# Optimization experiments

Measured on AMD Instinct MI355X. Metric: run time of the kernel, lower is better.

## Reference

```python
import jax, jax.numpy as jnp
import numpy as np

LATENT_DIM = 256
CODEBOOK_SIZE = 8192
COMMITMENT_WEIGHT = 0.25
CODEBOOK_WEIGHT = 1.0


def setup_inputs() -> dict:
    key = jax.random.key(0)
    k1, k2 = jax.random.split(key)
    latents = jax.random.normal(k1, (16, 1024, LATENT_DIM), dtype=jnp.float32)
    patch_mask = jnp.ones((16, 1024), dtype=jnp.float32)
    # nn.init.uniform_(codebook.weight, -1/K, 1/K)
    codebook = jax.random.uniform(
        k2, (CODEBOOK_SIZE, LATENT_DIM), dtype=jnp.float32,
        minval=-1.0 / CODEBOOK_SIZE, maxval=1.0 / CODEBOOK_SIZE)
    return {"latents": latents, "patch_mask": patch_mask, "codebook": codebook}


def reference(latents, patch_mask, codebook):
    B, P, D = latents.shape
    flat = latents.reshape(-1, D)  # [N, D]
    # squared euclidean distances [N, K]
    distances = (
        jnp.sum(flat * flat, axis=1, keepdims=True)
        + jnp.sum(codebook * codebook, axis=1)
        - 2.0 * flat @ codebook.T
    )
    symbol_ids = jnp.argmin(distances, axis=1)          # [N]
    quantized = codebook[symbol_ids].reshape(B, P, D)   # [B, P, D]
    symbol_ids = symbol_ids.reshape(B, P)

    st_quantized = latents + jax.lax.stop_gradient(quantized - latents)
    commitment_loss = jnp.mean((latents - jax.lax.stop_gradient(quantized)) ** 2) * COMMITMENT_WEIGHT
    codebook_loss = jnp.mean((quantized - jax.lax.stop_gradient(latents)) ** 2) * CODEBOOK_WEIGHT

    # perplexity: masked codeword usage histogram without materializing one-hot
    denom = jnp.maximum(jnp.sum(patch_mask), 1.0)
    avg_probs = jax.ops.segment_sum(
        patch_mask.reshape(-1), symbol_ids.reshape(-1),
        num_segments=CODEBOOK_SIZE) / denom
    perplexity = jnp.exp(-jnp.sum(avg_probs * jnp.log(avg_probs + 1e-8)))

    return symbol_ids, quantized, st_quantized, commitment_loss, codebook_loss, perplexity
```

## Files before the change

kernel.cpp:

```cpp
#include <hip/hip_runtime.h>
#include <math.h>

#define DD 256
#define KK 8192
#define NN 16384
#define MT 32
#define RPW 8
#define NT 512
#define NCH (KK / NT)
#define DT 8
#define NSL (DD / DT)
#define NEPOCH (NCH * NSL)
#define NBLOCKS (NN / MT)
#define CBUFF 4096
#define RSTRIDE 260

#define OUT_IDS   0
#define OUT_Q     16384
#define OUT_ST    4210688
#define OUT_COMMIT 8404992
#define OUT_CBL    8404993
#define OUT_PERP   8404994

__device__ __forceinline__ void gl2lds16(const float* g, float* l) {
    __builtin_amdgcn_global_load_lds(
        (const __attribute__((address_space(1))) float*)g,
        (__attribute__((address_space(3))) float*)l, 16, 0, 0);
}

__device__ __forceinline__ float rlane(float v, int l) {
    return __int_as_float(__builtin_amdgcn_readlane(__float_as_int(v), l));
}

__device__ __forceinline__ float np_block128_sumsq(const float* p) {
    #pragma clang fp contract(off)
    float r0 = p[0] * p[0], r1 = p[1] * p[1], r2 = p[2] * p[2], r3 = p[3] * p[3];
    float r4 = p[4] * p[4], r5 = p[5] * p[5], r6 = p[6] * p[6], r7 = p[7] * p[7];
    for (int i = 8; i < 128; i += 8) {
        r0 = r0 + p[i + 0] * p[i + 0];
        r1 = r1 + p[i + 1] * p[i + 1];
        r2 = r2 + p[i + 2] * p[i + 2];
        r3 = r3 + p[i + 3] * p[i + 3];
        r4 = r4 + p[i + 4] * p[i + 4];
        r5 = r5 + p[i + 5] * p[i + 5];
        r6 = r6 + p[i + 6] * p[i + 6];
        r7 = r7 + p[i + 7] * p[i + 7];
    }
    return ((r0 + r1) + (r2 + r3)) + ((r4 + r5) + (r6 + r7));
}

__device__ __forceinline__ float np_pairwise256_sumsq(const float* a) {
    #pragma clang fp contract(off)
    float s0 = np_block128_sumsq(a);
    float s1 = np_block128_sumsq(a + 128);
    return s0 + s1;
}

__global__ __launch_bounds__(256) void rowsumsq(const float* __restrict__ A,
                                                float* __restrict__ out) {
    __shared__ __align__(16) float sA[64][RSTRIDE];
    const int tid = threadIdx.x;
    const int base = blockIdx.x * 64;
    #pragma unroll
    for (int i = 0; i < 16; ++i) {
        int g = i * 256 + tid;
        int row = g >> 6, d4 = g & 63;
        float4 v = reinterpret_cast<const float4*>(A)[(size_t)(base + row) * (DD / 4) + d4];
        *reinterpret_cast<float4*>(&sA[row][d4 * 4]) = v;
    }
    __syncthreads();
    if (tid < 64) out[base + tid] = np_pairwise256_sumsq(sA[tid]);
}

__global__ __launch_bounds__(256, 2) void vq_main(const float* __restrict__ X,
                                                  const float* __restrict__ CB,
                                                  const float* __restrict__ c2,
                                                  const float* __restrict__ x2,
                                                  const float* __restrict__ mask,
                                                  float* __restrict__ out,
                                                  float* __restrict__ hist,
                                                  float* __restrict__ partial) {
    __shared__ __align__(16) float sX[8192];
    __shared__ __align__(16) float sC[2 * CBUFF];
    __shared__ int   row_id[MT];
    __shared__ float wsum[4];

    const int tid  = threadIdx.x;
    const int lane = tid & 63;
    const int wid  = tid >> 6;
    const int widu = __builtin_amdgcn_readfirstlane(wid);
    const int block_row = blockIdx.x * MT;

    {
        const unsigned rr = lane & 7u, d4r = lane >> 3;
        #pragma unroll
        for (int k = 0; k < 8; ++k)
            gl2lds16(X + (size_t)(block_row + widu * 8 + rr) * DD + k * 32 + d4r * 4,
                     &sX[(widu * 8 + k) * 256]);
    }

    unsigned coff[4];
    #pragma unroll
    for (int k = 0; k < 4; ++k) {
        unsigned u  = (widu * 4u + (unsigned)k) * 64u + (unsigned)lane;
        unsigned c  = u & 511u;
        unsigned pl = u >> 9;
        coff[k] = c * DD + pl * 4u;
    }
    #pragma unroll
    for (int k = 0; k < 4; ++k)
        gl2lds16(CB + coff[k], &sC[(widu * 4 + k) * 256]);

    float x2r[RPW];
    #pragma unroll
    for (int rr = 0; rr < RPW; ++rr) x2r[rr] = x2[block_row + wid * RPW + rr];

    __syncthreads();

    float best[RPW];
    int   besti[RPW];
    #pragma unroll
    for (int rr = 0; rr < RPW; ++rr) { best[rr] = 3.4e38f; besti[rr] = 0; }

    for (int ch = 0; ch < NCH; ++ch) {
        float c2v[8];
        #pragma unroll
        for (int j = 0; j < 8; ++j) c2v[j] = c2[ch * NT + lane + 64 * j];

        float acc[8][8];
        #pragma unroll
        for (int rr = 0; rr < 8; ++rr)
            #pragma unroll
            for (int j = 0; j < 8; ++j) acc[rr][j] = 0.0f;

        float4 xp;

        #pragma unroll 4
        for (int sl = 0; sl < NSL; ++sl) {
            const int e = ch * NSL + sl;

            if (e + 1 < NEPOCH) {
                const int nch = (e + 1) >> 5, nsl = (e + 1) & 31;
                const float* so = CB + (size_t)nch * (NT * DD) + nsl * DT;
                float* dst = &sC[((e + 1) & 1) * CBUFF];
                #pragma unroll
                for (int k = 0; k < 4; ++k)
                    gl2lds16(so + coff[k], dst + (widu * 4 + k) * 256);
            }

            if ((sl & 3) == 0) {
                const int b = sl >> 2;
                xp = *reinterpret_cast<const float4*>(&sX[(wid * 8 + b) * 256 + lane * 4]);
            }

            const float* cb_ = &sC[(e & 1) * CBUFF] + lane * 4;
            #pragma unroll
            for (int s = 0; s < 2; ++s) {
                const int t = (sl & 3) * 2 + s;
                float4 cc[8];
                #pragma unroll
                for (int j = 0; j < 8; ++j)
                    cc[j] = *reinterpret_cast<const float4*>(cb_ + s * 2048 + j * 256);
                #pragma unroll
                for (int rr = 0; rr < 8; ++rr) {
                    const int rl = t * 8 + rr;
                    const float sx = rlane(xp.x, rl);
                    const float sy = rlane(xp.y, rl);
                    const float sz = rlane(xp.z, rl);
                    const float sw = rlane(xp.w, rl);
                    #pragma unroll
                    for (int j = 0; j < 8; ++j) {
                        acc[rr][j] = fmaf(sx, cc[j].x, acc[rr][j]);
                        acc[rr][j] = fmaf(sy, cc[j].y, acc[rr][j]);
                        acc[rr][j] = fmaf(sz, cc[j].z, acc[rr][j]);
                        acc[rr][j] = fmaf(sw, cc[j].w, acc[rr][j]);
                    }
                }
            }
            __syncthreads();
        }

        #pragma unroll
        for (int rr = 0; rr < 8; ++rr) {
            #pragma unroll
            for (int j = 0; j < 8; ++j) {
                const int col = ch * NT + lane + 64 * j;
                float t1 = x2r[rr] + c2v[j];
                float sc = t1 - 2.0f * acc[rr][j];
                if (sc < best[rr] || (sc == best[rr] && col < besti[rr])) {
                    best[rr] = sc; besti[rr] = col;
                }
            }
        }
    }

    #pragma unroll
    for (int rr = 0; rr < RPW; ++rr) {
        float b = best[rr];
        int  bi = besti[rr];
        #pragma unroll
        for (int m = 32; m > 0; m >>= 1) {
            float b2 = __shfl_xor(b, m, 64);
            int   i2 = __shfl_xor(bi, m, 64);
            if (b2 < b || (b2 == b && i2 < bi)) { b = b2; bi = i2; }
        }
        if (lane == 0) row_id[wid * RPW + rr] = bi;
    }
    __syncthreads();

    if (tid < MT) {
        int bi = row_id[tid];
        out[OUT_IDS + block_row + tid] = (float)bi;
        atomicAdd(&hist[bi], mask[block_row + tid]);
    }

    float msep = 0.0f;
    float* outq  = out + OUT_Q;
    float* outst = out + OUT_ST;
    #pragma unroll
    for (int i = 0; i < 8; ++i) {
        int g = i * 256 + tid;
        int row = g >> 6;
        int d4  = g & 63;
        int id  = row_id[row];
        float4 q = reinterpret_cast<const float4*>(CB)[(size_t)id * (DD / 4) + d4];
        float4 x = reinterpret_cast<const float4*>(X)[(size_t)(block_row + row) * (DD / 4) + d4];
        float4 st;
        st.x = x.x + (q.x - x.x);
        st.y = x.y + (q.y - x.y);
        st.z = x.z + (q.z - x.z);
        st.w = x.w + (q.w - x.w);
        float dx = x.x - q.x; msep = fmaf(dx, dx, msep);
        dx = x.y - q.y; msep = fmaf(dx, dx, msep);
        dx = x.z - q.z; msep = fmaf(dx, dx, msep);
        dx = x.w - q.w; msep = fmaf(dx, dx, msep);
        size_t o = (size_t)(block_row + row) * (DD / 4) + d4;
        reinterpret_cast<float4*>(outq)[o]  = q;
        reinterpret_cast<float4*>(outst)[o] = st;
    }
    #pragma unroll
    for (int off = 32; off > 0; off >>= 1) msep += __shfl_down(msep, off, 64);
    if (lane == 0) wsum[wid] = msep;
    __syncthreads();
    if (tid == 0) partial[blockIdx.x] = wsum[0] + wsum[1] + wsum[2] + wsum[3];
}

__global__ __launch_bounds__(256) void vq_finalize(const float* __restrict__ partial,
                                                   const float* __restrict__ hist,
                                                   float* __restrict__ out) {
    __shared__ double red[256];
    const int tid = threadIdx.x;

    double ps = 0.0;
    for (int j = tid; j < NBLOCKS; j += 256) ps += (double)partial[j];
    red[tid] = ps;
    __syncthreads();
    for (int s = 128; s > 0; s >>= 1) {
        if (tid < s) red[tid] += red[tid + s];
        __syncthreads();
    }
    double mse_sum = red[0];
    __syncthreads();

    double hs = 0.0;
    for (int j = tid; j < KK; j += 256) hs += (double)hist[j];
    red[tid] = hs;
    __syncthreads();
    for (int s = 128; s > 0; s >>= 1) {
        if (tid < s) red[tid] += red[tid + s];
        __syncthreads();
    }
    double denom = red[0] > 1.0 ? red[0] : 1.0;
    __syncthreads();

    double ent = 0.0;
    for (int j = tid; j < KK; j += 256) {
        double p = (double)hist[j] / denom;
        ent += p * log(p + 1e-8);
    }
    red[tid] = ent;
    __syncthreads();
    for (int s = 128; s > 0; s >>= 1) {
        if (tid < s) red[tid] += red[tid + s];
        __syncthreads();
    }

    if (tid == 0) {
        double mse = mse_sum / (double)((size_t)NN * DD);
        out[OUT_COMMIT] = (float)(mse * 0.25);
        out[OUT_CBL]    = (float)mse;
        out[OUT_PERP]   = (float)exp(-red[0]);
    }
}

extern "C" void kernel_launch(void* const* d_in, const int* in_sizes, int n_in,
                              void* d_out, int out_size, void* d_ws, size_t ws_size,
                              hipStream_t stream) {
    const float* latents = (const float*)d_in[0];
    const float* mask    = (const float*)d_in[1];
    const float* cb      = (const float*)d_in[2];
    float* out = (float*)d_out;

    float* hist    = (float*)d_ws;
    float* partial = hist + KK;
    float* c2      = partial + NBLOCKS;
    float* x2      = c2 + KK;

    hipMemsetAsync(d_ws, 0, KK * sizeof(float), stream);
    rowsumsq<<<KK / 64, 256, 0, stream>>>(cb, c2);
    rowsumsq<<<NN / 64, 256, 0, stream>>>(latents, x2);
    vq_main<<<NBLOCKS, 256, 0, stream>>>(latents, cb, c2, x2, mask, out, hist, partial);
    vq_finalize<<<1, 256, 0, stream>>>(partial, hist, out);
}
```

Baseline: 1.133 ms.

## Split codebook across two wave groups per block and merge argmin in LDS

```diff
diff --git a/kernel.cpp b/kernel.cpp
--- a/kernel.cpp
+++ b/kernel.cpp
@@ -7,12 +7,12 @@
 #define MT 32
 #define RPW 8
 #define NT 512
-#define NCH (KK / NT)
-#define DT 8
+#define NCHG 8
+#define DT 4
 #define NSL (DD / DT)
-#define NEPOCH (NCH * NSL)
+#define NEPG (NCHG * NSL)
 #define NBLOCKS (NN / MT)
-#define CBUFF 4096
+#define CBUFF 2048
 #define RSTRIDE 260
 
 #define OUT_IDS   0
@@ -72,7 +72,7 @@
     if (tid < 64) out[base + tid] = np_pairwise256_sumsq(sA[tid]);
 }
 
-__global__ __launch_bounds__(256, 2) void vq_main(const float* __restrict__ X,
+__global__ __launch_bounds__(512, 4) void vq_main(const float* __restrict__ X,
                                                   const float* __restrict__ CB,
                                                   const float* __restrict__ c2,
                                                   const float* __restrict__ x2,
@@ -81,7 +81,9 @@
                                                   float* __restrict__ hist,
                                                   float* __restrict__ partial) {
     __shared__ __align__(16) float sX[8192];
-    __shared__ __align__(16) float sC[2 * CBUFF];
+    __shared__ __align__(16) float sC[4 * CBUFF];
+    __shared__ float gbest[2][MT];
+    __shared__ int   gidx[2][MT];
     __shared__ int   row_id[MT];
     __shared__ float wsum[4];
 
@@ -89,31 +91,37 @@
     const int lane = tid & 63;
     const int wid  = tid >> 6;
     const int widu = __builtin_amdgcn_readfirstlane(wid);
+    const int g    = wid >> 2;
+    const int gu   = widu >> 2;
+    const int wg   = wid & 3;
+    const int wgu  = widu & 3;
     const int block_row = blockIdx.x * MT;
 
     {
         const unsigned rr = lane & 7u, d4r = lane >> 3;
-        #pragma unroll
-        for (int k = 0; k < 8; ++k)
-            gl2lds16(X + (size_t)(block_row + widu * 8 + rr) * DD + k * 32 + d4r * 4,
-                     &sX[(widu * 8 + k) * 256]);
-    }
-
-    unsigned coff[4];
-    #pragma unroll
-    for (int k = 0; k < 4; ++k) {
-        unsigned u  = (widu * 4u + (unsigned)k) * 64u + (unsigned)lane;
-        unsigned c  = u & 511u;
-        unsigned pl = u >> 9;
-        coff[k] = c * DD + pl * 4u;
-    }
-    #pragma unroll
-    for (int k = 0; k < 4; ++k)
-        gl2lds16(CB + coff[k], &sC[(widu * 4 + k) * 256]);
+        const int r8 = widu >> 1, h = widu & 1;
+        #pragma unroll
+        for (int k = 0; k < 4; ++k) {
+            const int kk = h * 4 + k;
+            gl2lds16(X + (size_t)(block_row + r8 * 8 + rr) * DD + kk * 32 + d4r * 4,
+                     &sX[(r8 * 8 + kk) * 256]);
+        }
+    }
+
+    unsigned coff[2];
+    #pragma unroll
+    for (int k = 0; k < 2; ++k)
+        coff[k] = ((wgu * 2u + (unsigned)k) * 64u + (unsigned)lane) * DD;
+
+    const float* CBg = CB + (size_t)gu * NCHG * NT * DD;
+    float* sCg = &sC[gu * 2 * CBUFF];
+    #pragma unroll
+    for (int k = 0; k < 2; ++k)
+        gl2lds16(CBg + coff[k], sCg + (wgu * 2 + k) * 256);
 
     float x2r[RPW];
     #pragma unroll
-    for (int rr = 0; rr < RPW; ++rr) x2r[rr] = x2[block_row + wid * RPW + rr];
+    for (int rr = 0; rr < RPW; ++rr) x2r[rr] = x2[block_row + wg * RPW + rr];
 
     __syncthreads();
 
@@ -122,10 +130,11 @@
     #pragma unroll
     for (int rr = 0; rr < RPW; ++rr) { best[rr] = 3.4e38f; besti[rr] = 0; }
 
-    for (int ch = 0; ch < NCH; ++ch) {
+    for (int ch = 0; ch < NCHG; ++ch) {
+        const int chg = g * NCHG + ch;
         float c2v[8];
         #pragma unroll
-        for (int j = 0; j < 8; ++j) c2v[j] = c2[ch * NT + lane + 64 * j];
+        for (int j = 0; j < 8; ++j) c2v[j] = c2[chg * NT + lane + 64 * j];
 
         float acc[8][8];
         #pragma unroll
@@ -135,46 +144,42 @@
 
         float4 xp;
 
-        #pragma unroll 4
+        #pragma unroll 8
         for (int sl = 0; sl < NSL; ++sl) {
             const int e = ch * NSL + sl;
 
-            if (e + 1 < NEPOCH) {
-                const int nch = (e + 1) >> 5, nsl = (e + 1) & 31;
-                const float* so = CB + (size_t)nch * (NT * DD) + nsl * DT;
-                float* dst = &sC[((e + 1) & 1) * CBUFF];
+            if (e + 1 < NEPG) {
+                const int nch = (e + 1) >> 6, nsl = (e + 1) & 63;
+                const float* so = CBg + (size_t)nch * (NT * DD) + nsl * DT;
+                float* dst = sCg + ((e + 1) & 1) * CBUFF;
                 #pragma unroll
-                for (int k = 0; k < 4; ++k)
-                    gl2lds16(so + coff[k], dst + (widu * 4 + k) * 256);
+                for (int k = 0; k < 2; ++k)
+                    gl2lds16(so + coff[k], dst + (wgu * 2 + k) * 256);
             }
 
-            if ((sl & 3) == 0) {
-                const int b = sl >> 2;
-                xp = *reinterpret_cast<const float4*>(&sX[(wid * 8 + b) * 256 + lane * 4]);
-            }
-
-            const float* cb_ = &sC[(e & 1) * CBUFF] + lane * 4;
+            if ((sl & 7) == 0)
+                xp = *reinterpret_cast<const float4*>(
+                        &sX[(wg * 8 + (sl >> 3)) * 256 + lane * 4]);
+
+            const int t = sl & 7;
+            const float* cb_ = sCg + (e & 1) * CBUFF + lane * 4;
+            float4 cc[8];
             #pragma unroll
-            for (int s = 0; s < 2; ++s) {
-                const int t = (sl & 3) * 2 + s;
-                float4 cc[8];
+            for (int j = 0; j < 8; ++j)
+                cc[j] = *reinterpret_cast<const float4*>(cb_ + j * 256);
+            #pragma unroll
+            for (int rr = 0; rr < 8; ++rr) {
+                const int rl = t * 8 + rr;
+                const float sx = rlane(xp.x, rl);
+                const float sy = rlane(xp.y, rl);
+                const float sz = rlane(xp.z, rl);
+                const float sw = rlane(xp.w, rl);
                 #pragma unroll
-                for (int j = 0; j < 8; ++j)
-                    cc[j] = *reinterpret_cast<const float4*>(cb_ + s * 2048 + j * 256);
-                #pragma unroll
-                for (int rr = 0; rr < 8; ++rr) {
-                    const int rl = t * 8 + rr;
-                    const float sx = rlane(xp.x, rl);
-                    const float sy = rlane(xp.y, rl);
-                    const float sz = rlane(xp.z, rl);
-                    const float sw = rlane(xp.w, rl);
-                    #pragma unroll
-                    for (int j = 0; j < 8; ++j) {
-                        acc[rr][j] = fmaf(sx, cc[j].x, acc[rr][j]);
-                        acc[rr][j] = fmaf(sy, cc[j].y, acc[rr][j]);
-                        acc[rr][j] = fmaf(sz, cc[j].z, acc[rr][j]);
-                        acc[rr][j] = fmaf(sw, cc[j].w, acc[rr][j]);
-                    }
+                for (int j = 0; j < 8; ++j) {
+                    acc[rr][j] = fmaf(sx, cc[j].x, acc[rr][j]);
+                    acc[rr][j] = fmaf(sy, cc[j].y, acc[rr][j]);
+                    acc[rr][j] = fmaf(sz, cc[j].z, acc[rr][j]);
+                    acc[rr][j] = fmaf(sw, cc[j].w, acc[rr][j]);
                 }
             }
             __syncthreads();
@@ -184,7 +189,7 @@
         for (int rr = 0; rr < 8; ++rr) {
             #pragma unroll
             for (int j = 0; j < 8; ++j) {
-                const int col = ch * NT + lane + 64 * j;
+                const int col = chg * NT + lane + 64 * j;
                 float t1 = x2r[rr] + c2v[j];
                 float sc = t1 - 2.0f * acc[rr][j];
                 if (sc < best[rr] || (sc == best[rr] && col < besti[rr])) {
@@ -204,43 +209,51 @@
             int   i2 = __shfl_xor(bi, m, 64);
             if (b2 < b || (b2 == b && i2 < bi)) { b = b2; bi = i2; }
         }
-        if (lane == 0) row_id[wid * RPW + rr] = bi;
+        if (lane == 0) {
+            gbest[g][wg * RPW + rr] = b;
+            gidx [g][wg * RPW + rr] = bi;
+        }
     }
     __syncthreads();
 
     if (tid < MT) {
-        int bi = row_id[tid];
+        const float b0 = gbest[0][tid], b1 = gbest[1][tid];
+        const int bi = (b1 < b0) ? gidx[1][tid] : gidx[0][tid];
+        row_id[tid] = bi;
         out[OUT_IDS + block_row + tid] = (float)bi;
         atomicAdd(&hist[bi], mask[block_row + tid]);
     }
-
-    float msep = 0.0f;
-    float* outq  = out + OUT_Q;
-    float* outst = out + OUT_ST;
-    #pragma unroll
-    for (int i = 0; i < 8; ++i) {
-        int g = i * 256 + tid;
-        int row = g >> 6;
-        int d4  = g & 63;
-        int id  = row_id[row];
-        float4 q = reinterpret_cast<const float4*>(CB)[(size_t)id * (DD / 4) + d4];
-        float4 x = reinterpret_cast<const float4*>(X)[(size_t)(block_row + row) * (DD / 4) + d4];
-        float4 st;
-        st.x = x.x + (q.x - x.x);
-        st.y = x.y + (q.y - x.y);
-        st.z = x.z + (q.z - x.z);
-        st.w = x.w + (q.w - x.w);
-        float dx = x.x - q.x; msep = fmaf(dx, dx, msep);
-        dx = x.y - q.y; msep = fmaf(dx, dx, msep);
-        dx = x.z - q.z; msep = fmaf(dx, dx, msep);
-        dx = x.w - q.w; msep = fmaf(dx, dx, msep);
-        size_t o = (size_t)(block_row + row) * (DD / 4) + d4;
-        reinterpret_cast<float4*>(outq)[o]  = q;
-        reinterpret_cast<float4*>(outst)[o] = st;
-    }
-    #pragma unroll
-    for (int off = 32; off > 0; off >>= 1) msep += __shfl_down(msep, off, 64);
-    if (lane == 0) wsum[wid] = msep;
+    __syncthreads();
+
+    if (tid < 256) {
+        float msep = 0.0f;
+        float* outq  = out + OUT_Q;
+        float* outst = out + OUT_ST;
+        #pragma unroll
+        for (int i = 0; i < 8; ++i) {
+            int g2 = i * 256 + tid;
+            int row = g2 >> 6;
+            int d4  = g2 & 63;
+            int id  = row_id[row];
+            float4 q = reinterpret_cast<const float4*>(CB)[(size_t)id * (DD / 4) + d4];
+            float4 x = reinterpret_cast<const float4*>(X)[(size_t)(block_row + row) * (DD / 4) + d4];
+            float4 st;
+            st.x = x.x + (q.x - x.x);
+            st.y = x.y + (q.y - x.y);
+            st.z = x.z + (q.z - x.z);
+            st.w = x.w + (q.w - x.w);
+            float dx = x.x - q.x; msep = fmaf(dx, dx, msep);
+            dx = x.y - q.y; msep = fmaf(dx, dx, msep);
+            dx = x.z - q.z; msep = fmaf(dx, dx, msep);
+            dx = x.w - q.w; msep = fmaf(dx, dx, msep);
+            size_t o = (size_t)(block_row + row) * (DD / 4) + d4;
+            reinterpret_cast<float4*>(outq)[o]  = q;
+            reinterpret_cast<float4*>(outst)[o] = st;
+        }
+        #pragma unroll
+        for (int off = 32; off > 0; off >>= 1) msep += __shfl_down(msep, off, 64);
+        if (lane == 0) wsum[wid] = msep;
+    }
     __syncthreads();
     if (tid == 0) partial[blockIdx.x] = wsum[0] + wsum[1] + wsum[2] + wsum[3];
 }
@@ -309,6 +322,6 @@
     hipMemsetAsync(d_ws, 0, KK * sizeof(float), stream);
     rowsumsq<<<KK / 64, 256, 0, stream>>>(cb, c2);
     rowsumsq<<<NN / 64, 256, 0, stream>>>(latents, x2);
-    vq_main<<<NBLOCKS, 256, 0, stream>>>(latents, cb, c2, x2, mask, out, hist, partial);
+    vq_main<<<NBLOCKS, 512, 0, stream>>>(latents, cb, c2, x2, mask, out, hist, partial);
     vq_finalize<<<1, 256, 0, stream>>>(partial, hist, out);
 }
```

Result: slower. 1.389 ms (+22.6%).
